# Optimization experiments

Measured on AMD Instinct MI355X. Metric: run time of the kernel, lower is better.

The kernel has to match this reference:

```python
import jax, jax.numpy as jnp
import numpy as np

# GraphConvolutionSparse forward:
#   x = sparse_dropout(X)            (dropout=0.0 -> identity, kept faithful)
#   h = X @ W                        (sparse-dense matmul via segment_sum)
#   h = A @ h                        (sparse-dense matmul via segment_sum)
#   out = relu(h)

DROPOUT = 0.0  # layer default; keep_prob = 1 - dropout

def setup_inputs() -> dict:
    key = jax.random.key(0)
    k1, k2, k3, k4, k5, k6, k7 = jax.random.split(key, 7)
    N = 100000       # nodes
    D_IN = 512       # input feature dim
    D_OUT = 128      # output feature dim
    NNZ_X = 800000   # nonzeros in sparse feature matrix
    N_E = 1600000    # adjacency nonzeros (edges)
    x_vals = jax.random.normal(k1, (NNZ_X,), dtype=jnp.float32)
    x_rows = jax.random.randint(k2, (NNZ_X,), 0, N, dtype=jnp.int32)
    x_cols = jax.random.randint(k3, (NNZ_X,), 0, D_IN, dtype=jnp.int32)
    adj_vals = jax.random.uniform(k4, (N_E,), dtype=jnp.float32)
    adj_rows = jax.random.randint(k5, (N_E,), 0, N, dtype=jnp.int32)
    adj_cols = jax.random.randint(k6, (N_E,), 0, N, dtype=jnp.int32)
    init_range = np.sqrt(6.0 / (D_IN + D_OUT)).astype(np.float32)
    W = jax.random.uniform(k7, (D_IN, D_OUT), minval=-init_range, maxval=init_range, dtype=jnp.float32)
    return {"x_vals": x_vals, "x_rows": x_rows, "x_cols": x_cols,
            "adj_vals": adj_vals, "adj_rows": adj_rows, "adj_cols": adj_cols,
            "W": W, "n_nodes": N}

def reference(x_vals, x_rows, x_cols, adj_vals, adj_rows, adj_cols, W, n_nodes):
    keep_prob = 1.0 - DROPOUT
    # sparse dropout: with dropout=0.0 the mask keeps all entries and scale is 1,
    # so it reduces to the deterministic identity (faithful to tf semantics).
    vals = x_vals * (1.0 / keep_prob)
    # h = X @ W : gather weight rows by feature column, scale, scatter-add by node row
    xw = jax.ops.segment_sum(vals[:, None] * W[x_cols], x_rows, num_segments=n_nodes)  # [N, D_OUT]
    # out = A @ h : gather source-node rows, scale by edge weight, scatter-add to dest
    agg = jax.ops.segment_sum(adj_vals[:, None] * xw[adj_cols], adj_rows, num_segments=n_nodes)  # [N, D_OUT]
    return jax.nn.relu(agg)
```

## Files before the change

### kernel.cpp

```cpp
#include <hip/hip_runtime.h>
#include <hip/hip_fp16.h>


#define DOUT 128
#define RBB 128
#define RBB_BITS 7
#define NKEY 128
#define NBMAX 4096
#define COLMASK 131071
#define CTH 512
#define NW 8
#define CAPX 1536
#define CAPA 3072
#define SCB 8192

static inline size_t align_up(size_t x, size_t a) { return (x + a - 1) & ~(a - 1); }

__device__ inline int2 nt_load_int2(const int2* p) {
    long long v = __builtin_nontemporal_load((const long long*)p);
    int2 r; r.x = (int)(unsigned int)(v & 0xffffffffLL); r.y = (int)(v >> 32);
    return r;
}
__device__ inline void nt_store_float2(float2* p, float2 v) {
    union { float2 f; long long l; } u; u.f = v;
    __builtin_nontemporal_store(u.l, (long long*)p);
}

__device__ inline int wave_incl_scan(int v, int lane) {
    #pragma unroll
    for (int off = 1; off < 64; off <<= 1) {
        int up = __shfl_up(v, off, 64);
        if (lane >= off) v += up;
    }
    return v;
}

__global__ __launch_bounds__(256) void prep_kernel(int* __restrict__ cnts, int ncnt,
                                                   const float* __restrict__ W,
                                                   __half2* __restrict__ Wh, int whtot) {
    int i = blockIdx.x * 256 + threadIdx.x;
    if (i < ncnt) cnts[i] = 0;
    if (i < whtot) {
        int c = i >> 6, l = i & 63;
        Wh[i] = __floats2half2_rn(W[(c << 7) + 2 * l], W[(c << 7) + 2 * l + 1]);
    }
}

__global__ __launch_bounds__(256) void hist_coarse(const int* __restrict__ xr, int nx,
                                                   const int* __restrict__ ar, int na,
                                                   int* __restrict__ cx, int* __restrict__ ca) {
    __shared__ int h[2 * NBMAX];
    for (int i = threadIdx.x; i < 2 * NBMAX; i += 256) h[i] = 0;
    __syncthreads();
    int base = blockIdx.x * 4096;
    int tot = nx + na;
    #pragma unroll
    for (int k = 0; k < 16; ++k) {
        int i = base + k * 256 + threadIdx.x;
        if (i < tot) {
            if (i < nx) atomicAdd(&h[xr[i] >> RBB_BITS], 1);
            else        atomicAdd(&h[NBMAX + (ar[i - nx] >> RBB_BITS)], 1);
        }
    }
    __syncthreads();
    for (int i = threadIdx.x; i < 2 * NBMAX; i += 256) {
        int c = h[i];
        if (c) {
            if (i < NBMAX) atomicAdd(&cx[i], c);
            else           atomicAdd(&ca[i - NBMAX], c);
        }
    }
}

__global__ __launch_bounds__(1024) void scan_nb(const int* __restrict__ cx, const int* __restrict__ ca,
                                                int* __restrict__ bx, int* __restrict__ ba,
                                                int* __restrict__ curx, int* __restrict__ cura, int nb) {
    const int* c = blockIdx.x ? ca : cx;
    int* bs  = blockIdx.x ? ba : bx;
    int* cur = blockIdx.x ? cura : curx;
    __shared__ int wsum[16];
    __shared__ int woff[16];
    __shared__ int carry_s, chunk_tot;
    int tid = threadIdx.x, lane = tid & 63, wid = tid >> 6;
    if (tid == 0) carry_s = 0;
    __syncthreads();
    for (int base = 0; base < nb; base += 1024) {
        int i = base + tid;
        int v = (i < nb) ? c[i] : 0;
        int incl = wave_incl_scan(v, lane);
        if (lane == 63) wsum[wid] = incl;
        __syncthreads();
        if (wid == 0 && lane < 16) {
            int s = wsum[lane];
            int is = s;
            #pragma unroll
            for (int off = 1; off < 16; off <<= 1) {
                int up = __shfl_up(is, off, 64);
                if (lane >= off) is += up;
            }
            woff[lane] = is - s;
            if (lane == 15) chunk_tot = is;
        }
        __syncthreads();
        int excl = incl - v + woff[wid] + carry_s;
        if (i < nb) { bs[i] = excl; cur[i] = excl; }
        __syncthreads();
        if (tid == 0) carry_s += chunk_tot;
        __syncthreads();
    }
    if (tid == 0) bs[nb] = carry_s;
}

__global__ __launch_bounds__(512) void bucket_scatter2(const int* __restrict__ xr, const int* __restrict__ xc,
                                                       const float* __restrict__ xv, int nx,
                                                       const int* __restrict__ ar, const int* __restrict__ ac,
                                                       const float* __restrict__ av, int na,
                                                       int* __restrict__ curx, int* __restrict__ cura,
                                                       int2* __restrict__ stx, int2* __restrict__ sta,
                                                       int nb, int nblk_x, int capx, int capa) {
    const int* rows; const int* cols; const float* vals; int n;
    int* gcur; int2* stage; int base; int cap;
    if (blockIdx.x < nblk_x) {
        rows = xr; cols = xc; vals = xv; n = nx; gcur = curx; stage = stx;
        base = blockIdx.x * SCB; cap = capx;
    } else {
        rows = ar; cols = ac; vals = av; n = na; gcur = cura; stage = sta;
        base = (blockIdx.x - nblk_x) * SCB; cap = capa;
    }
    __shared__ int h[NBMAX];
    __shared__ int bcur[NBMAX];
    for (int i = threadIdx.x; i < nb; i += 512) h[i] = 0;
    __syncthreads();
    int rr[16]; int cc[16]; float vv[16];
    #pragma unroll
    for (int k = 0; k < 16; ++k) {
        int i = base + k * 512 + threadIdx.x;
        rr[k] = -1;
        if (i < n) {
            rr[k] = __builtin_nontemporal_load(&rows[i]);
            cc[k] = __builtin_nontemporal_load(&cols[i]);
            vv[k] = __builtin_nontemporal_load(&vals[i]);
            atomicAdd(&h[rr[k] >> RBB_BITS], 1);
        }
    }
    __syncthreads();
    for (int b = threadIdx.x; b < nb; b += 512) {
        int c = h[b];
        if (c) {
            int r = atomicAdd(&gcur[b], c);
            bcur[b] = (cap > 0) ? (b * cap + r) : r;
        }
    }
    __syncthreads();
    #pragma unroll
    for (int k = 0; k < 16; ++k) {
        if (rr[k] >= 0) {
            int b = rr[k] >> RBB_BITS;
            int p = atomicAdd(&bcur[b], 1);
            if (cap == 0 || p < b * cap + cap)
                stage[p] = make_int2(((rr[k] & (RBB - 1)) << 17) | cc[k], __float_as_int(vv[k]));
        }
    }
}


__global__ __launch_bounds__(CTH) void consumer_xw(const int* __restrict__ bx, const int* __restrict__ gcnt,
                                                   const int2* __restrict__ stage,
                                                   const __half2* __restrict__ Wh, __half2* __restrict__ xwh,
                                                   int N, int cap) {
    __shared__ int2 sp[CAPX];
    __shared__ int hoff[NKEY + 1];
    __shared__ int curs[NKEY];
    int b = blockIdx.x;
    int s, cnt;
    if (cap > 0) { s = b * cap; cnt = min(gcnt[b], cap); }
    else         { s = bx[b]; cnt = bx[b + 1] - s; }
    int tid = threadIdx.x, lane = tid & 63, wid = tid >> 6;
    bool fast = (cnt <= CAPX);
    if (tid < NKEY) curs[tid] = 0;
    __syncthreads();
    int2 pr[3];
    if (fast) {
        #pragma unroll
        for (int k = 0; k < 3; ++k) {
            int i = k * CTH + tid;
            if (i < cnt) {
                pr[k] = nt_load_int2(&stage[s + i]);
                atomicAdd(&curs[(pr[k].x >> 17) & (NKEY - 1)], 1);
            }
        }
    }
    __syncthreads();
    if (wid == 0) {
        int carry = 0;
        #pragma unroll
        for (int q = 0; q < 2; ++q) {
            int k = (q << 6) + lane;
            int v = curs[k];
            int incl = wave_incl_scan(v, lane) + carry;
            hoff[k] = incl - v;
            curs[k] = incl - v;
            carry = __shfl(incl, 63, 64);
        }
        if (lane == 0) hoff[NKEY] = carry;
    }
    __syncthreads();
    if (fast) {
        #pragma unroll
        for (int k = 0; k < 3; ++k) {
            int i = k * CTH + tid;
            if (i < cnt) {
                int r = (pr[k].x >> 17) & (NKEY - 1);
                sp[atomicAdd(&curs[r], 1)] = pr[k];
            }
        }
    }
    __syncthreads();
    int row0 = b << RBB_BITS;
    #pragma unroll 1
    for (int rr = 0; rr < NKEY / NW; ++rr) {
        int r = wid + rr * NW;
        int grow = row0 + r;
        if (grow >= N) continue;
        float ax = 0.f, ay = 0.f;
        if (fast) {
            int j = hoff[r], o1 = hoff[r + 1];
            for (; j + 3 < o1; j += 4) {
                int2 c0 = sp[j], c1 = sp[j + 1], c2 = sp[j + 2], c3 = sp[j + 3];
                float2 w0 = __half22float2(Wh[((size_t)(c0.x & COLMASK) << 6) + lane]);
                float2 w1 = __half22float2(Wh[((size_t)(c1.x & COLMASK) << 6) + lane]);
                float2 w2 = __half22float2(Wh[((size_t)(c2.x & COLMASK) << 6) + lane]);
                float2 w3 = __half22float2(Wh[((size_t)(c3.x & COLMASK) << 6) + lane]);
                float v0 = __int_as_float(c0.y), v1 = __int_as_float(c1.y);
                float v2 = __int_as_float(c2.y), v3 = __int_as_float(c3.y);
                ax += v0 * w0.x + v1 * w1.x + v2 * w2.x + v3 * w3.x;
                ay += v0 * w0.y + v1 * w1.y + v2 * w2.y + v3 * w3.y;
            }
            for (; j < o1; ++j) {
                int2 c0 = sp[j];
                float2 w0 = __half22float2(Wh[((size_t)(c0.x & COLMASK) << 6) + lane]);
                float v0 = __int_as_float(c0.y);
                ax += v0 * w0.x; ay += v0 * w0.y;
            }
        } else {
            for (int j = 0; j < cnt; ++j) {
                int2 c0 = stage[s + j];
                if (((c0.x >> 17) & (NKEY - 1)) == r) {
                    float2 w0 = __half22float2(Wh[((size_t)(c0.x & COLMASK) << 6) + lane]);
                    float v0 = __int_as_float(c0.y);
                    ax += v0 * w0.x; ay += v0 * w0.y;
                }
            }
        }
        xwh[((size_t)grow << 6) + lane] = __float22half2_rn(make_float2(ax, ay));
    }
}

__global__ __launch_bounds__(CTH) void consumer_adj(const int* __restrict__ ba, const int* __restrict__ gcnt,
                                                    const int2* __restrict__ stage,
                                                    const __half2* __restrict__ xwh, float* __restrict__ out,
                                                    int N, int cap) {
    __shared__ int2 sp[CAPA];
    __shared__ int hoff[NKEY + 1];
    __shared__ int curs[NKEY];
    int b = blockIdx.x;
    int s, cnt;
    if (cap > 0) { s = b * cap; cnt = min(gcnt[b], cap); }
    else         { s = ba[b]; cnt = ba[b + 1] - s; }
    int tid = threadIdx.x, lane = tid & 63, wid = tid >> 6;
    bool fast = (cnt <= CAPA);
    if (tid < NKEY) curs[tid] = 0;
    __syncthreads();
    int2 pr[6];
    if (fast) {
        #pragma unroll
        for (int k = 0; k < 6; ++k) {
            int i = k * CTH + tid;
            if (i < cnt) {
                pr[k] = nt_load_int2(&stage[s + i]);
                atomicAdd(&curs[(pr[k].x >> 17) & (NKEY - 1)], 1);
            }
        }
    }
    __syncthreads();
    if (wid == 0) {
        int carry = 0;
        #pragma unroll
        for (int q = 0; q < 2; ++q) {
            int k = (q << 6) + lane;
            int v = curs[k];
            int incl = wave_incl_scan(v, lane) + carry;
            hoff[k] = incl - v;
            curs[k] = incl - v;
            carry = __shfl(incl, 63, 64);
        }
        if (lane == 0) hoff[NKEY] = carry;
    }
    __syncthreads();
    if (fast) {
        #pragma unroll
        for (int k = 0; k < 6; ++k) {
            int i = k * CTH + tid;
            if (i < cnt) {
                int r = (pr[k].x >> 17) & (NKEY - 1);
                sp[atomicAdd(&curs[r], 1)] = pr[k];
            }
        }
    }
    __syncthreads();
    int row0 = b << RBB_BITS;
    #pragma unroll 1
    for (int rr = 0; rr < NKEY / NW; ++rr) {
        int r = wid + rr * NW;
        int grow = row0 + r;
        if (grow >= N) continue;
        float ax = 0.f, ay = 0.f;
        if (fast) {
            int j = hoff[r], o1 = hoff[r + 1];
            for (; j + 3 < o1; j += 4) {
                int2 c0 = sp[j], c1 = sp[j + 1], c2 = sp[j + 2], c3 = sp[j + 3];
                float2 h0 = __half22float2(xwh[((size_t)(c0.x & COLMASK) << 6) + lane]);
                float2 h1 = __half22float2(xwh[((size_t)(c1.x & COLMASK) << 6) + lane]);
                float2 h2 = __half22float2(xwh[((size_t)(c2.x & COLMASK) << 6) + lane]);
                float2 h3 = __half22float2(xwh[((size_t)(c3.x & COLMASK) << 6) + lane]);
                float v0 = __int_as_float(c0.y), v1 = __int_as_float(c1.y);
                float v2 = __int_as_float(c2.y), v3 = __int_as_float(c3.y);
                ax += v0 * h0.x + v1 * h1.x + v2 * h2.x + v3 * h3.x;
                ay += v0 * h0.y + v1 * h1.y + v2 * h2.y + v3 * h3.y;
            }
            for (; j < o1; ++j) {
                int2 c0 = sp[j];
                float2 h0 = __half22float2(xwh[((size_t)(c0.x & COLMASK) << 6) + lane]);
                float v0 = __int_as_float(c0.y);
                ax += v0 * h0.x; ay += v0 * h0.y;
            }
        } else {
            for (int j = 0; j < cnt; ++j) {
                int2 c0 = stage[s + j];
                if (((c0.x >> 17) & (NKEY - 1)) == r) {
                    float2 h0 = __half22float2(xwh[((size_t)(c0.x & COLMASK) << 6) + lane]);
                    float v0 = __int_as_float(c0.y);
                    ax += v0 * h0.x; ay += v0 * h0.y;
                }
            }
        }
        nt_store_float2(&((float2*)(out + (size_t)grow * DOUT))[lane],
                        make_float2(fmaxf(ax, 0.f), fmaxf(ay, 0.f)));
    }
}

__global__ void spmm_xw_atomic(const float* __restrict__ x_vals, const int* __restrict__ x_rows,
                               const int* __restrict__ x_cols, const float* __restrict__ W,
                               float* __restrict__ xw, int nnz) {
    long long t = (long long)blockIdx.x * blockDim.x + threadIdx.x;
    int i = (int)(t >> 7), d = (int)(t & 127);
    if (i >= nnz) return;
    atomicAdd(&xw[(long long)x_rows[i] * DOUT + d], x_vals[i] * W[(long long)x_cols[i] * DOUT + d]);
}
__global__ void spmm_adj_atomic(const float* __restrict__ adj_vals, const int* __restrict__ adj_rows,
                                const int* __restrict__ adj_cols, const float* __restrict__ xw,
                                float* __restrict__ out, int n_e) {
    long long t = (long long)blockIdx.x * blockDim.x + threadIdx.x;
    int e = (int)(t >> 7), d = (int)(t & 127);
    if (e >= n_e) return;
    atomicAdd(&out[(long long)adj_rows[e] * DOUT + d], adj_vals[e] * xw[(long long)adj_cols[e] * DOUT + d]);
}
__global__ void relu_kernel(float4* __restrict__ out, int n4) {
    int i = blockIdx.x * blockDim.x + threadIdx.x;
    if (i >= n4) return;
    float4 v = out[i];
    v.x = fmaxf(v.x, 0.f); v.y = fmaxf(v.y, 0.f);
    v.z = fmaxf(v.z, 0.f); v.w = fmaxf(v.w, 0.f);
    out[i] = v;
}

extern "C" void kernel_launch(void* const* d_in, const int* in_sizes, int n_in,
                              void* d_out, int out_size, void* d_ws, size_t ws_size,
                              hipStream_t stream) {
    const float* x_vals   = (const float*)d_in[0];
    const int*   x_rows   = (const int*)d_in[1];
    const int*   x_cols   = (const int*)d_in[2];
    const float* adj_vals = (const float*)d_in[3];
    const int*   adj_rows = (const int*)d_in[4];
    const int*   adj_cols = (const int*)d_in[5];
    const float* W        = (const float*)d_in[6];
    float* out = (float*)d_out;

    const int nnz_x = in_sizes[0];
    const int n_e   = in_sizes[3];
    const int N     = out_size / DOUT;
    const int D_IN  = in_sizes[6] / DOUT;
    const int nbc   = (N + RBB - 1) / RBB;

    char* ws = (char*)d_ws;
    size_t off = 0;
    size_t xw_off   = off; off = align_up(off + (size_t)N * DOUT * sizeof(__half), 128);
    size_t wh_off   = off; off = align_up(off + (size_t)D_IN * 64 * sizeof(__half2), 128);
    size_t cx_off   = off; off += (size_t)NBMAX * sizeof(int);
    size_t ca_off   = off; off = align_up(off + (size_t)NBMAX * sizeof(int), 128);
    size_t bx_off   = off; off = align_up(off + (size_t)(NBMAX + 1) * sizeof(int), 128);
    size_t baoff    = off; off = align_up(off + (size_t)(NBMAX + 1) * sizeof(int), 128);
    size_t head = off;
    size_t sxc_off = head;
    size_t sac_off = align_up(sxc_off + (size_t)nbc * CAPX * sizeof(int2), 128);
    size_t needed_cap = align_up(sac_off + (size_t)nbc * CAPA * sizeof(int2), 128);
    size_t sxm_off = head;
    size_t sam_off = align_up(sxm_off + (size_t)nnz_x * sizeof(int2), 128);
    size_t needed_mid = align_up(sam_off + (size_t)n_e * sizeof(int2), 128);

    bool ok_dims = (nbc <= NBMAX) && (N <= (COLMASK + 1));
    const int ncnt = 2 * NBMAX;
    const int whtot = D_IN * 64;
    const int prep_n = (ncnt > whtot ? ncnt : whtot);

    if (ok_dims && ws_size >= needed_cap) {
        __half2* xwh  = (__half2*)(ws + xw_off);
        __half2* Wh   = (__half2*)(ws + wh_off);
        int*  cx      = (int*)(ws + cx_off);
        int*  ca      = (int*)(ws + ca_off);
        int2* stage_x = (int2*)(ws + sxc_off);
        int2* stage_a = (int2*)(ws + sac_off);

        prep_kernel<<<(prep_n + 255) / 256, 256, 0, stream>>>(cx, ncnt, W, Wh, whtot);

        int nblk_x = (nnz_x + SCB - 1) / SCB;
        int nblk_a = (n_e + SCB - 1) / SCB;
        bucket_scatter2<<<nblk_x + nblk_a, 512, 0, stream>>>(x_rows, x_cols, x_vals, nnz_x,
                                                             adj_rows, adj_cols, adj_vals, n_e,
                                                             cx, ca, stage_x, stage_a,
                                                             nbc, nblk_x, CAPX, CAPA);
        consumer_xw<<<nbc, CTH, 0, stream>>>(nullptr, cx, stage_x, Wh, xwh, N, CAPX);
        consumer_adj<<<nbc, CTH, 0, stream>>>(nullptr, ca, stage_a, xwh, out, N, CAPA);
    } else if (ok_dims && ws_size >= needed_mid) {
        __half2* xwh  = (__half2*)(ws + xw_off);
        __half2* Wh   = (__half2*)(ws + wh_off);
        int*  cx      = (int*)(ws + cx_off);
        int*  ca      = (int*)(ws + ca_off);
        int*  bx      = (int*)(ws + bx_off);
        int*  ba      = (int*)(ws + baoff);
        int2* stage_x = (int2*)(ws + sxm_off);
        int2* stage_a = (int2*)(ws + sam_off);

        prep_kernel<<<(prep_n + 255) / 256, 256, 0, stream>>>(cx, ncnt, W, Wh, whtot);

        int tot = nnz_x + n_e;
        hist_coarse<<<(tot + 4095) / 4096, 256, 0, stream>>>(x_rows, nnz_x, adj_rows, n_e, cx, ca);
        scan_nb<<<2, 1024, 0, stream>>>(cx, ca, bx, ba, cx, ca, nbc);

        int nblk_x = (nnz_x + SCB - 1) / SCB;
        int nblk_a = (n_e + SCB - 1) / SCB;
        bucket_scatter2<<<nblk_x + nblk_a, 512, 0, stream>>>(x_rows, x_cols, x_vals, nnz_x,
                                                             adj_rows, adj_cols, adj_vals, n_e,
                                                             cx, ca, stage_x, stage_a,
                                                             nbc, nblk_x, 0, 0);
        consumer_xw<<<nbc, CTH, 0, stream>>>(bx, nullptr, stage_x, Wh, xwh, N, 0);
        consumer_adj<<<nbc, CTH, 0, stream>>>(ba, nullptr, stage_a, xwh, out, N, 0);
    } else {
        float* xw = (float*)ws;
        hipMemsetAsync(xw, 0, (size_t)out_size * sizeof(float), stream);
        hipMemsetAsync(out, 0, (size_t)out_size * sizeof(float), stream);
        long long t1 = (long long)nnz_x * DOUT;
        spmm_xw_atomic<<<(int)((t1 + 255) / 256), 256, 0, stream>>>(x_vals, x_rows, x_cols, W, xw, nnz_x);
        long long t2 = (long long)n_e * DOUT;
        spmm_adj_atomic<<<(int)((t2 + 255) / 256), 256, 0, stream>>>(adj_vals, adj_rows, adj_cols, xw, out, n_e);
        relu_kernel<<<(out_size / 4 + 255) / 256, 256, 0, stream>>>((float4*)out, out_size / 4);
    }
}
```

Before: 207.5 us.

## Locally sort bucket scatter in shared memory before coalesced global writes

The bucket scatter kernel now counting-sorts its chunk of entries by row bucket in LDS: it builds a histogram, does a wave prefix scan for local offsets, reserves global slots with one atomic per bucket, and then writes the sorted entries out contiguously. Before, each entry went directly to a scattered global address. Adjacent threads now write consecutive slots within a bucket, which is meant to improve store coalescing. The chunk size per block is halved to fit the LDS staging buffer. The cost is more LDS usage, an extra scan and synchronization, and a limit of 1024 buckets (N up to 131072), since larger N takes the fallback path.

```diff
diff --git a/kernel.cpp b/kernel.cpp
--- a/kernel.cpp
+++ b/kernel.cpp
@@ -6,13 +6,14 @@
 #define RBB 128
 #define RBB_BITS 7
 #define NKEY 128
+#define NBIN 1024
 #define NBMAX 4096
 #define COLMASK 131071
 #define CTH 512
 #define NW 8
 #define CAPX 1536
 #define CAPA 3072
-#define SCB 8192
+#define SCB 4096
 
 static inline size_t align_up(size_t x, size_t a) { return (x + a - 1) & ~(a - 1); }
 
@@ -127,38 +128,68 @@
         rows = ar; cols = ac; vals = av; n = na; gcur = cura; stage = sta;
         base = (blockIdx.x - nblk_x) * SCB; cap = capa;
     }
-    __shared__ int h[NBMAX];
-    __shared__ int bcur[NBMAX];
-    for (int i = threadIdx.x; i < nb; i += 512) h[i] = 0;
-    __syncthreads();
-    int rr[16]; int cc[16]; float vv[16];
+    __shared__ int2 sp[SCB];
+    __shared__ unsigned short bin16[SCB];
+    __shared__ int cnt[NBIN];
+    __shared__ int lbase[NBIN];
+    __shared__ int gb[NBIN];
+    __shared__ int tot_s;
+    int tid = threadIdx.x, lane = tid & 63, wid = tid >> 6;
+    for (int i = tid; i < NBIN; i += 512) cnt[i] = 0;
+    __syncthreads();
+    int rr[8]; int cc[8]; float vv[8];
     #pragma unroll
-    for (int k = 0; k < 16; ++k) {
-        int i = base + k * 512 + threadIdx.x;
+    for (int k = 0; k < 8; ++k) {
+        int i = base + k * 512 + tid;
         rr[k] = -1;
         if (i < n) {
             rr[k] = __builtin_nontemporal_load(&rows[i]);
             cc[k] = __builtin_nontemporal_load(&cols[i]);
             vv[k] = __builtin_nontemporal_load(&vals[i]);
-            atomicAdd(&h[rr[k] >> RBB_BITS], 1);
-        }
-    }
-    __syncthreads();
-    for (int b = threadIdx.x; b < nb; b += 512) {
-        int c = h[b];
-        if (c) {
-            int r = atomicAdd(&gcur[b], c);
-            bcur[b] = (cap > 0) ? (b * cap + r) : r;
-        }
+            atomicAdd(&cnt[rr[k] >> RBB_BITS], 1);
+        }
+    }
+    __syncthreads();
+    if (wid == 0) {
+        int carry = 0;
+        #pragma unroll
+        for (int q = 0; q < NBIN / 64; ++q) {
+            int k = (q << 6) + lane;
+            int v = cnt[k];
+            int incl = wave_incl_scan(v, lane) + carry;
+            lbase[k] = incl - v;
+            carry = __shfl(incl, 63, 64);
+        }
+        if (lane == 0) tot_s = carry;
+    }
+    __syncthreads();
+    for (int b = tid; b < nb; b += 512) {
+        int c = cnt[b];
+        if (c) gb[b] = atomicAdd(&gcur[b], c);
+        cnt[b] = lbase[b];
     }
     __syncthreads();
     #pragma unroll
-    for (int k = 0; k < 16; ++k) {
+    for (int k = 0; k < 8; ++k) {
         if (rr[k] >= 0) {
             int b = rr[k] >> RBB_BITS;
-            int p = atomicAdd(&bcur[b], 1);
-            if (cap == 0 || p < b * cap + cap)
-                stage[p] = make_int2(((rr[k] & (RBB - 1)) << 17) | cc[k], __float_as_int(vv[k]));
+            int p = atomicAdd(&cnt[b], 1);
+            sp[p] = make_int2(((rr[k] & (RBB - 1)) << 17) | cc[k], __float_as_int(vv[k]));
+            bin16[p] = (unsigned short)b;
+        }
+    }
+    __syncthreads();
+    int tot = tot_s;
+    for (int p = tid; p < tot; p += 512) {
+        int2 e = sp[p];
+        int b = bin16[p];
+        int q = p - lbase[b];
+        int r = gb[b];
+        if (cap > 0) {
+            int slot = r + q;
+            if (slot < cap) stage[b * cap + slot] = e;
+        } else {
+            stage[r + q] = e;
         }
     }
 }
@@ -408,7 +439,7 @@
     size_t sam_off = align_up(sxm_off + (size_t)nnz_x * sizeof(int2), 128);
     size_t needed_mid = align_up(sam_off + (size_t)n_e * sizeof(int2), 128);
 
-    bool ok_dims = (nbc <= NBMAX) && (N <= (COLMASK + 1));
+    bool ok_dims = (nbc <= NBIN) && (N <= (COLMASK + 1));
     const int ncnt = 2 * NBMAX;
     const int whtot = D_IN * 64;
     const int prep_n = (ncnt > whtot ? ncnt : whtot);
```

New measurement: 201.6 us (median of 2 runs). 2.8% less time.
